# Optimization experiments

Measured on AMD Instinct MI355X. Metric: run time of the kernel, lower is better.

The kernel has to match this reference:

```python
import jax, jax.numpy as jnp
import numpy as np

N_PAPER, N_AUTHOR = 200000, 100000
D_PAPER, D_AUTHOR = 128, 64
H, OUT = 64, 32
E_CITES, E_WRITES = 4000000, 2000000


def _gcn(x, W, b, src, dst, n):
    # GCNConv with default add_self_loops=True, symmetric normalization
    xl = x @ W
    deg = jnp.zeros((n,), xl.dtype).at[dst].add(1.0) + 1.0  # +1 for self loop
    dis = jax.lax.rsqrt(deg)
    norm = dis[src] * dis[dst]
    out = jax.ops.segment_sum(xl[src] * norm[:, None], dst, num_segments=n)
    out = out + xl * (dis * dis)[:, None]  # self-loop term: norm_ii = 1/deg_i
    return out + b


def _sage(x_src, x_dst, Wl, bl, Wr, src, dst, n_dst):
    # SAGEConv: mean neighbor aggregation -> lin_l, plus root lin_r on dst
    ones = jnp.ones(src.shape, x_src.dtype)
    cnt = jnp.maximum(jax.ops.segment_sum(ones, dst, num_segments=n_dst), 1.0)
    mean = jax.ops.segment_sum(x_src[src], dst, num_segments=n_dst) / cnt[:, None]
    return mean @ Wl + bl + x_dst @ Wr


def _gat(x_src, x_dst, Ws, Wd, a_s, a_d, b, src, dst, n_dst):
    # GATConv heads=1, bipartite, add_self_loops=False, leaky_relu slope 0.2
    xs = x_src @ Ws  # [Ns, H]
    xd = x_dst @ Wd  # [Nd, H]
    a_src = xs @ a_s  # [Ns]
    a_dst = xd @ a_d  # [Nd]
    e = a_src[src] + a_dst[dst]
    e = jnp.where(e > 0, e, 0.2 * e)
    m = jax.ops.segment_max(e, dst, num_segments=n_dst)
    m = jnp.where(jnp.isfinite(m), m, 0.0)  # nodes with no in-edges
    ex = jnp.exp(e - m[dst])
    denom = jax.ops.segment_sum(ex, dst, num_segments=n_dst)
    alpha = ex / denom[dst]
    out = jax.ops.segment_sum(alpha[:, None] * xs[src], dst, num_segments=n_dst)
    return out + b


def _forward(x_paper, x_author, params, cites_src, cites_dst, writes_src, writes_dst):
    for (gW, gb, sWl, sbl, sWr, aWs, aWd, aas, aad, ab) in params:
        p_gcn = _gcn(x_paper, gW, gb, cites_src, cites_dst, N_PAPER)
        p_sage = _sage(x_author, x_paper, sWl, sbl, sWr, writes_src, writes_dst, N_PAPER)
        # rev_writes: paper -> author, i.e. src=writes_dst (paper), dst=writes_src (author)
        a_gat = _gat(x_paper, x_author, aWs, aWd, aas, aad, ab, writes_dst, writes_src, N_AUTHOR)
        x_paper = jax.nn.relu(p_gcn + p_sage)  # HeteroConv aggr='sum'
        x_author = jax.nn.relu(a_gat)
    return x_paper, x_author


def setup_inputs() -> dict:
    key = jax.random.key(0)
    ks = jax.random.split(key, 40)
    rn = lambda i, shp, s=0.1: jax.random.normal(ks[i], shp, jnp.float32) * s
    inp = {}
    inp['x_paper'] = rn(0, (N_PAPER, D_PAPER), 1.0)
    inp['x_author'] = rn(1, (N_AUTHOR, D_AUTHOR), 1.0)
    dims = [(D_PAPER, D_AUTHOR), (H, H)]
    i = 2
    for l, (dp, da) in enumerate(dims):
        inp[f'gcn_W{l}'] = rn(i, (dp, H)); i += 1
        inp[f'gcn_b{l}'] = jnp.zeros((H,), jnp.float32)
        inp[f'sage_Wl{l}'] = rn(i, (da, H)); i += 1
        inp[f'sage_bl{l}'] = jnp.zeros((H,), jnp.float32)
        inp[f'sage_Wr{l}'] = rn(i, (dp, H)); i += 1
        inp[f'gat_Ws{l}'] = rn(i, (dp, H)); i += 1
        inp[f'gat_Wd{l}'] = rn(i, (da, H)); i += 1
        inp[f'gat_as{l}'] = rn(i, (H,)); i += 1
        inp[f'gat_ad{l}'] = rn(i, (H,)); i += 1
        inp[f'gat_b{l}'] = jnp.zeros((H,), jnp.float32)
    inp['lin_W'] = rn(i, (H, OUT)); i += 1
    inp['lin_b'] = jnp.zeros((OUT,), jnp.float32)
    inp['cites_src'] = jax.random.randint(ks[30], (E_CITES,), 0, N_PAPER)
    inp['cites_dst'] = jax.random.randint(ks[31], (E_CITES,), 0, N_PAPER)
    inp['writes_src'] = jax.random.randint(ks[32], (E_WRITES,), 0, N_AUTHOR)
    inp['writes_dst'] = jax.random.randint(ks[33], (E_WRITES,), 0, N_PAPER)
    return inp


def reference(x_paper, x_author,
              gcn_W0, gcn_b0, sage_Wl0, sage_bl0, sage_Wr0,
              gat_Ws0, gat_Wd0, gat_as0, gat_ad0, gat_b0,
              gcn_W1, gcn_b1, sage_Wl1, sage_bl1, sage_Wr1,
              gat_Ws1, gat_Wd1, gat_as1, gat_ad1, gat_b1,
              lin_W, lin_b,
              cites_src, cites_dst, writes_src, writes_dst):
    params = [
        (gcn_W0, gcn_b0, sage_Wl0, sage_bl0, sage_Wr0, gat_Ws0, gat_Wd0, gat_as0, gat_ad0, gat_b0),
        (gcn_W1, gcn_b1, sage_Wl1, sage_bl1, sage_Wr1, gat_Ws1, gat_Wd1, gat_as1, gat_ad1, gat_b1),
    ]
    _, x_author_out = _forward(x_paper, x_author, params, cites_src, cites_dst, writes_src, writes_dst)
    return x_author_out @ lin_W + lin_b
```

## Files before the change

kernel.cpp:

```cpp
#include <hip/hip_runtime.h>
#include <hip/hip_bf16.h>

#define NP 200000
#define NA 100000
#define DP 128
#define HD 64
#define EC 4000000
#define EW 2000000
#define NSCAN (2 * NP + NA)
#define NBUCK 4
#define CAPC 64
#define CAPW 48
#define CAPA 64

typedef __hip_bfloat16 bf16;
typedef __attribute__((ext_vector_type(8))) short short8;
typedef __attribute__((ext_vector_type(4))) float f32x4;

__device__ __forceinline__ float bf2f(bf16 h) { return __bfloat162float(h); }

__device__ __forceinline__ short8 pack8(float4 a, float4 b) {
    union {
        short8 s;
        unsigned u[4];
    } r;
    __hip_bfloat162 h;
    h = __float22bfloat162_rn(float2{a.x, a.y});
    r.u[0] = *reinterpret_cast<unsigned*>(&h);
    h = __float22bfloat162_rn(float2{a.z, a.w});
    r.u[1] = *reinterpret_cast<unsigned*>(&h);
    h = __float22bfloat162_rn(float2{b.x, b.y});
    r.u[2] = *reinterpret_cast<unsigned*>(&h);
    h = __float22bfloat162_rn(float2{b.z, b.w});
    r.u[3] = *reinterpret_cast<unsigned*>(&h);
    return r.s;
}


__global__ __launch_bounds__(256) void fill_pass_kernel(const int* __restrict__ cs,
                                                        const int* __restrict__ cd,
                                                        const int* __restrict__ ws,
                                                        const int* __restrict__ wd,
                                                        int* __restrict__ CUR,
                                                        int* __restrict__ colC,
                                                        int* __restrict__ colWd,
                                                        int* __restrict__ colWa, int bucket) {
    long i = (long)blockIdx.x * 256 + threadIdx.x;
    if (i < EC) {
        int d = __builtin_nontemporal_load(&cd[i]);
        if ((int)(((long)d * NBUCK) / NP) != bucket) return;
        int s = __builtin_nontemporal_load(&cs[i]);
        int pos = atomicAdd(&CUR[d * 4], 1);
        if (pos < CAPC) colC[(size_t)d * CAPC + pos] = s;
    } else if (i < (long)EC + EW) {
        long e = i - EC;
        int d = __builtin_nontemporal_load(&wd[e]);
        int a = __builtin_nontemporal_load(&ws[e]);
        if ((int)(((long)d * NBUCK) / NP) == bucket) {
            int pos = atomicAdd(&CUR[(NP + d) * 4], 1);
            if (pos < CAPW) colWd[(size_t)d * CAPW + pos] = a;
        }
        if ((int)(((long)a * NBUCK) / NA) == bucket) {
            int pos = atomicAdd(&CUR[(2 * NP + a) * 4], 1);
            if (pos < CAPA) colWa[(size_t)a * CAPA + pos] = d;
        }
    }
}

__global__ __launch_bounds__(256) void finalize_kernel(const int* __restrict__ CUR,
                                                       float* __restrict__ dis,
                                                       float* __restrict__ invc) {
    int i = blockIdx.x * 256 + threadIdx.x;
    if (i >= NP) return;
    dis[i] = rsqrtf((float)CUR[i * 4] + 1.0f);
    invc[i] = 1.0f / fmaxf((float)CUR[(NP + i) * 4], 1.0f);
}


__global__ __launch_bounds__(256) void conv_author_kernel(const float* __restrict__ XA,
                                                          const float* __restrict__ wvec,
                                                          bf16* __restrict__ XAbf,
                                                          float* __restrict__ adst) {
    __shared__ float vs[64];
    if (threadIdx.x < 64) vs[threadIdx.x] = wvec[threadIdx.x];
    __syncthreads();
    int r = blockIdx.x * 4 + (threadIdx.x >> 6);
    int lane = threadIdx.x & 63;
    float x = XA[(size_t)r * 64 + lane];
    XAbf[(size_t)r * 64 + lane] = __float2bfloat16(x);
    float p = x * vs[lane];
#pragma unroll
    for (int o = 32; o > 0; o >>= 1) p += __shfl_xor(p, o, 64);
    if (lane == 0) adst[r] = p;
}


__global__ void wprep_kernel(const float* __restrict__ Wg, const float* __restrict__ Wl,
                             const float* __restrict__ Wr, const float* __restrict__ Ws0,
                             const float* __restrict__ Ws1, short* __restrict__ WF,
                             const float* __restrict__ Wd0, const float* __restrict__ ad0,
                             const float* __restrict__ Wd1, const float* __restrict__ ad1,
                             float* __restrict__ wvec0, float* __restrict__ wvec1) {
    int bid = blockIdx.x;
    int lane = threadIdx.x;
    if (bid >= 64) {
        const float* Wd = (bid == 64) ? Wd0 : Wd1;
        const float* ad = (bid == 64) ? ad0 : ad1;
        float* wv = (bid == 64) ? wvec0 : wvec1;
        float s = 0.f;
        for (int c = 0; c < 64; c++) s += Wd[lane * 64 + c] * ad[c];
        wv[lane] = s;
        return;
    }
    int q = lane & 15, g = lane >> 4;
    int m, r;
    size_t dst;
    if (bid < 16) {
        m = 0; r = bid; dst = 0;
    } else if (bid < 40) {
        m = 1; r = bid - 16; dst = 8192;
    } else if (bid < 56) {
        m = 2; r = bid - 40; dst = 20480;
    } else {
        m = 3; r = bid - 56; dst = 28672;
    }
    int ks = r >> 2, n = r & 3;
    int col = n * 16 + q;
    float v[8];
#pragma unroll
    for (int j = 0; j < 8; j++) {
        int kr = ks * 32 + g * 8 + j;
        float x;
        if (m == 0) x = Wg[(size_t)kr * 64 + col];
        else if (m == 1) x = (kr < 64) ? Wl[(size_t)kr * 64 + col] : Wr[(size_t)(kr - 64) * 64 + col];
        else if (m == 2) x = Ws0[(size_t)kr * 64 + col];
        else x = Ws1[(size_t)kr * 64 + col];
        v[j] = x;
    }
    short8 s = pack8(float4{v[0], v[1], v[2], v[3]}, float4{v[4], v[5], v[6], v[7]});
    *reinterpret_cast<short8*>(WF + dst + ((size_t)r * 64 + lane) * 8) = s;
}


template <int K, int ASTRIDE, bool ABF16, bool ADOT, bool SCALE>
__global__ __launch_bounds__(256) void mfma_gemm_kernel(const void* __restrict__ Xv,
                                                        const short* __restrict__ Wf,
                                                        bf16* __restrict__ outb,
                                                        const float* __restrict__ avec,
                                                        float* __restrict__ adot,
                                                        const float* __restrict__ rowscale) {
    int tid = threadIdx.x;
    int lane = tid & 63, q = lane & 15, g = lane >> 4;
    int rw = blockIdx.x * 64 + (tid >> 6) * 16;
    int arow = rw + q;
    f32x4 acc[4];
#pragma unroll
    for (int n = 0; n < 4; n++) acc[n] = f32x4{0.f, 0.f, 0.f, 0.f};
#pragma unroll
    for (int ks = 0; ks < K / 32; ks++) {
        short8 af;
        if constexpr (ABF16) {
            af = *reinterpret_cast<const short8*>((const bf16*)Xv + (size_t)arow * ASTRIDE +
                                                  ks * 32 + g * 8);
        } else {
            const float* xr = (const float*)Xv + (size_t)arow * ASTRIDE + ks * 32 + g * 8;
            float4 a0 = *reinterpret_cast<const float4*>(xr);
            float4 a1 = *reinterpret_cast<const float4*>(xr + 4);
            af = pack8(a0, a1);
        }
#pragma unroll
        for (int n = 0; n < 4; n++) {
            short8 bfr =
                *reinterpret_cast<const short8*>(Wf + ((size_t)(ks * 4 + n) * 64 + lane) * 8);
            acc[n] = __builtin_amdgcn_mfma_f32_16x16x32_bf16(af, bfr, acc[n], 0, 0, 0);
        }
    }
    float av[4];
    if constexpr (ADOT) {
#pragma unroll
        for (int n = 0; n < 4; n++) av[n] = avec[n * 16 + q];
    }
#pragma unroll
    for (int j = 0; j < 4; j++) {
        int R = rw + g * 4 + j;
        float sc = 1.f;
        if constexpr (SCALE) sc = rowscale[R];
#pragma unroll
        for (int n = 0; n < 4; n++) {
            outb[(size_t)R * 64 + n * 16 + q] = __float2bfloat16(acc[n][j] * sc);
        }
        if constexpr (ADOT) {
            float t = acc[0][j] * av[0] + acc[1][j] * av[1] + acc[2][j] * av[2] + acc[3][j] * av[3];
            t += __shfl_xor(t, 1, 64);
            t += __shfl_xor(t, 2, 64);
            t += __shfl_xor(t, 4, 64);
            t += __shfl_xor(t, 8, 64);
            if (q == 0) adot[R] = t;
        }
    }
}


__global__ __launch_bounds__(256) void mfma_sage_kernel(const bf16* B3s,
                                                        const float* __restrict__ XP,
                                                        const float* __restrict__ B2,
                                                        const float* __restrict__ bl,
                                                        const short* __restrict__ Wf, bf16* P1) {
    int tid = threadIdx.x;
    int lane = tid & 63, q = lane & 15, g = lane >> 4;
    int rw = blockIdx.x * 64 + (tid >> 6) * 16;
    int arow = rw + q;
    f32x4 acc[4];
#pragma unroll
    for (int n = 0; n < 4; n++) acc[n] = f32x4{0.f, 0.f, 0.f, 0.f};
#pragma unroll
    for (int ks = 0; ks < 6; ks++) {
        short8 af;
        if (ks < 2) {
            af = *reinterpret_cast<const short8*>(B3s + (size_t)arow * 128 + 64 + ks * 32 + g * 8);
        } else {
            const float* xr = XP + (size_t)arow * DP + (ks - 2) * 32 + g * 8;
            float4 a0 = *reinterpret_cast<const float4*>(xr);
            float4 a1 = *reinterpret_cast<const float4*>(xr + 4);
            af = pack8(a0, a1);
        }
#pragma unroll
        for (int n = 0; n < 4; n++) {
            short8 bfr =
                *reinterpret_cast<const short8*>(Wf + ((size_t)(ks * 4 + n) * 64 + lane) * 8);
            acc[n] = __builtin_amdgcn_mfma_f32_16x16x32_bf16(af, bfr, acc[n], 0, 0, 0);
        }
    }
    float blv[4];
#pragma unroll
    for (int n = 0; n < 4; n++) blv[n] = bl[n * 16 + q];
#pragma unroll
    for (int j = 0; j < 4; j++) {
        int R = rw + g * 4 + j;
#pragma unroll
        for (int n = 0; n < 4; n++) {
            int col = n * 16 + q;
            float v = acc[n][j] + B2[(size_t)R * 64 + col] + blv[n];
            P1[(size_t)R * 128 + col] = __float2bfloat16(fmaxf(v, 0.f));
        }
    }
}


__global__ __launch_bounds__(256) void paper_gather_kernel(const bf16* __restrict__ B1,
                                                           const bf16* __restrict__ XA,
                                                           const int* __restrict__ CUR,
                                                           const int* colC,
                                                           const int* __restrict__ colWd,
                                                           const float* __restrict__ dis,
                                                           const float* __restrict__ invc,
                                                           const float* __restrict__ gb,
                                                           float* __restrict__ B2, bf16* B3s) {
    int node = __builtin_amdgcn_readfirstlane(blockIdx.x * 4 + (threadIdx.x >> 6));
    unsigned lane = threadIdx.x & 63;
    int degc = min(CUR[(unsigned)node * 4], CAPC);
    unsigned cb = (unsigned)node * CAPC;
    float dd = dis[(unsigned)node];
    float acc = bf2f(B1[((unsigned)node << 6) + lane]);
    int e = 0;
    for (; e + 8 <= degc; e += 8) {
        unsigned off[8];
#pragma unroll
        for (int j = 0; j < 8; j++) off[j] = ((unsigned)colC[cb + e + j] << 6) + lane;
        float v[8];
#pragma unroll
        for (int j = 0; j < 8; j++) v[j] = bf2f(B1[off[j]]);
#pragma unroll
        for (int j = 0; j < 8; j++) acc += v[j];
    }
    for (; e + 4 <= degc; e += 4) {
        unsigned o0 = ((unsigned)colC[cb + e] << 6) + lane;
        unsigned o1 = ((unsigned)colC[cb + e + 1] << 6) + lane;
        unsigned o2 = ((unsigned)colC[cb + e + 2] << 6) + lane;
        unsigned o3 = ((unsigned)colC[cb + e + 3] << 6) + lane;
        float v0 = bf2f(B1[o0]), v1 = bf2f(B1[o1]);
        float v2 = bf2f(B1[o2]), v3 = bf2f(B1[o3]);
        acc += v0 + v1;
        acc += v2 + v3;
    }
    for (; e < degc; e++) acc += bf2f(B1[((unsigned)colC[cb + e] << 6) + lane]);
    B2[((unsigned)node << 6) + lane] = acc * dd + gb[lane];
    int degw = min(CUR[((unsigned)NP + node) * 4], CAPW);
    unsigned wb = (unsigned)node * CAPW;
    float s = 0.f;
    e = 0;
    for (; e + 8 <= degw; e += 8) {
        unsigned off[8];
#pragma unroll
        for (int j = 0; j < 8; j++) off[j] = ((unsigned)colWd[wb + e + j] << 6) + lane;
        float v[8];
#pragma unroll
        for (int j = 0; j < 8; j++) v[j] = bf2f(XA[off[j]]);
#pragma unroll
        for (int j = 0; j < 8; j++) s += v[j];
    }
    for (; e + 4 <= degw; e += 4) {
        unsigned o0 = ((unsigned)colWd[wb + e] << 6) + lane;
        unsigned o1 = ((unsigned)colWd[wb + e + 1] << 6) + lane;
        unsigned o2 = ((unsigned)colWd[wb + e + 2] << 6) + lane;
        unsigned o3 = ((unsigned)colWd[wb + e + 3] << 6) + lane;
        float v0 = bf2f(XA[o0]), v1 = bf2f(XA[o1]);
        float v2 = bf2f(XA[o2]), v3 = bf2f(XA[o3]);
        s += v0 + v1;
        s += v2 + v3;
    }
    for (; e < degw; e++) s += bf2f(XA[((unsigned)colWd[wb + e] << 6) + lane]);
    B3s[(unsigned)node * 128u + 64u + lane] = __float2bfloat16(s * invc[(unsigned)node]);
}


__device__ __forceinline__ float lrelu(float v) { return v > 0.f ? v : 0.2f * v; }


__global__ __launch_bounds__(256) void gat_l0_kernel(const bf16* __restrict__ XS,
                                                     const int* __restrict__ CUR,
                                                     const int* __restrict__ colA,
                                                     const float* __restrict__ asrc,
                                                     float* __restrict__ adst,
                                                     const float* __restrict__ ab,
                                                     const float* __restrict__ wvec1) {
    int a = __builtin_amdgcn_readfirstlane(blockIdx.x * 4 + (threadIdx.x >> 6));
    unsigned lane = threadIdx.x & 63;
    int deg = min(CUR[(2u * NP + a) * 4], CAPA);
    unsigned cb = (unsigned)a * CAPA;
    float ada = adst[(unsigned)a];
    float acc = 0.f, den = 0.f;
    int e = 0;
    for (; e + 8 <= deg; e += 8) {
        unsigned p[8];
#pragma unroll
        for (int j = 0; j < 8; j++) p[j] = (unsigned)colA[cb + e + j];
        float x[8], v[8];
#pragma unroll
        for (int j = 0; j < 8; j++) x[j] = __expf(lrelu(asrc[p[j]] + ada));
#pragma unroll
        for (int j = 0; j < 8; j++) v[j] = bf2f(XS[(p[j] << 6) + lane]);
#pragma unroll
        for (int j = 0; j < 8; j++) {
            den += x[j];
            acc += x[j] * v[j];
        }
    }
    for (; e + 4 <= deg; e += 4) {
        unsigned p0 = (unsigned)colA[cb + e], p1 = (unsigned)colA[cb + e + 1];
        unsigned p2 = (unsigned)colA[cb + e + 2], p3 = (unsigned)colA[cb + e + 3];
        float x0 = __expf(lrelu(asrc[p0] + ada));
        float x1 = __expf(lrelu(asrc[p1] + ada));
        float x2 = __expf(lrelu(asrc[p2] + ada));
        float x3 = __expf(lrelu(asrc[p3] + ada));
        den += (x0 + x1) + (x2 + x3);
        acc += x0 * bf2f(XS[(p0 << 6) + lane]);
        acc += x1 * bf2f(XS[(p1 << 6) + lane]);
        acc += x2 * bf2f(XS[(p2 << 6) + lane]);
        acc += x3 * bf2f(XS[(p3 << 6) + lane]);
    }
    for (; e < deg; e++) {
        unsigned p = (unsigned)colA[cb + e];
        float x = __expf(lrelu(asrc[p] + ada));
        den += x;
        acc += x * bf2f(XS[(p << 6) + lane]);
    }
    float inv = den > 0.f ? 1.f / den : 0.f;
    float val = fmaxf(acc * inv + ab[lane], 0.f);
    float pr = val * wvec1[lane];
#pragma unroll
    for (int o = 32; o > 0; o >>= 1) pr += __shfl_xor(pr, o, 64);
    if (lane == 0) adst[(unsigned)a] = pr;
}


__global__ __launch_bounds__(256) void gat_final_kernel(const bf16* __restrict__ XS,
                                                        const int* __restrict__ CUR,
                                                        const int* __restrict__ colA,
                                                        const float* __restrict__ asrc,
                                                        const float* __restrict__ adst,
                                                        const float* __restrict__ ab,
                                                        const float* __restrict__ linW,
                                                        const float* __restrict__ linb,
                                                        float* __restrict__ out) {
    __shared__ float Ws[64 * 32];
    __shared__ float vbuf[4][64];
    __shared__ float lbs[32];
    int tid = threadIdx.x;
    for (int i = tid; i < 64 * 32; i += 256) Ws[i] = linW[i];
    if (tid < 32) lbs[tid] = linb[tid];
    __syncthreads();
    int wid = tid >> 6;
    int a = __builtin_amdgcn_readfirstlane(blockIdx.x * 4 + wid);
    unsigned lane = tid & 63;
    int deg = min(CUR[(2u * NP + a) * 4], CAPA);
    unsigned cb = (unsigned)a * CAPA;
    float ada = adst[(unsigned)a];
    float acc = 0.f, den = 0.f;
    int e = 0;
    for (; e + 8 <= deg; e += 8) {
        unsigned p[8];
#pragma unroll
        for (int j = 0; j < 8; j++) p[j] = (unsigned)colA[cb + e + j];
        float x[8], v[8];
#pragma unroll
        for (int j = 0; j < 8; j++) x[j] = __expf(lrelu(asrc[p[j]] + ada));
#pragma unroll
        for (int j = 0; j < 8; j++) v[j] = bf2f(XS[(p[j] << 6) + lane]);
#pragma unroll
        for (int j = 0; j < 8; j++) {
            den += x[j];
            acc += x[j] * v[j];
        }
    }
    for (; e + 4 <= deg; e += 4) {
        unsigned p0 = (unsigned)colA[cb + e], p1 = (unsigned)colA[cb + e + 1];
        unsigned p2 = (unsigned)colA[cb + e + 2], p3 = (unsigned)colA[cb + e + 3];
        float x0 = __expf(lrelu(asrc[p0] + ada));
        float x1 = __expf(lrelu(asrc[p1] + ada));
        float x2 = __expf(lrelu(asrc[p2] + ada));
        float x3 = __expf(lrelu(asrc[p3] + ada));
        den += (x0 + x1) + (x2 + x3);
        acc += x0 * bf2f(XS[(p0 << 6) + lane]);
        acc += x1 * bf2f(XS[(p1 << 6) + lane]);
        acc += x2 * bf2f(XS[(p2 << 6) + lane]);
        acc += x3 * bf2f(XS[(p3 << 6) + lane]);
    }
    for (; e < deg; e++) {
        unsigned p = (unsigned)colA[cb + e];
        float x = __expf(lrelu(asrc[p] + ada));
        den += x;
        acc += x * bf2f(XS[(p << 6) + lane]);
    }
    float inv = den > 0.f ? 1.f / den : 0.f;
    vbuf[wid][lane] = fmaxf(acc * inv + ab[lane], 0.f);
    __syncthreads();
    if (tid < 128) {
        int w = tid >> 5, c = tid & 31;
        int node = blockIdx.x * 4 + w;
        float s = lbs[c];
#pragma unroll
        for (int k = 0; k < 64; k++) s += vbuf[w][k] * Ws[k * 32 + c];
        out[(size_t)node * 32 + c] = s;
    }
}


static inline int cdivi(long a, long b) { return (int)((a + b - 1) / b); }

extern "C" void kernel_launch(void* const* d_in, const int* in_sizes, int n_in, void* d_out,
                              int out_size, void* d_ws, size_t ws_size, hipStream_t stream) {
    const float* x_paper = (const float*)d_in[0];
    const float* x_author = (const float*)d_in[1];
    const float* gcn_W0 = (const float*)d_in[2];
    const float* gcn_b0 = (const float*)d_in[3];
    const float* sage_Wl0 = (const float*)d_in[4];
    const float* sage_bl0 = (const float*)d_in[5];
    const float* sage_Wr0 = (const float*)d_in[6];
    const float* gat_Ws0 = (const float*)d_in[7];
    const float* gat_Wd0 = (const float*)d_in[8];
    const float* gat_as0 = (const float*)d_in[9];
    const float* gat_ad0 = (const float*)d_in[10];
    const float* gat_b0 = (const float*)d_in[11];
    const float* gat_Ws1 = (const float*)d_in[17];
    const float* gat_Wd1 = (const float*)d_in[18];
    const float* gat_as1 = (const float*)d_in[19];
    const float* gat_ad1 = (const float*)d_in[20];
    const float* gat_b1 = (const float*)d_in[21];
    const float* lin_W = (const float*)d_in[22];
    const float* lin_b = (const float*)d_in[23];
    const int* cites_src = (const int*)d_in[24];
    const int* cites_dst = (const int*)d_in[25];
    const int* writes_src = (const int*)d_in[26];
    const int* writes_dst = (const int*)d_in[27];

    float* out = (float*)d_out;

    char* base = (char*)d_ws;
    bf16* BF = (bf16*)base;
    base += (size_t)NP * 64 * 2;
    float* B2 = (float*)base;
    base += (size_t)NP * 64 * 4;
    int* colC = (int*)base;
    bf16* R3 = (bf16*)base;
    base += (size_t)NP * CAPC * 4;
    int* colWd = (int*)base;
    base += (size_t)NP * CAPW * 4;
    int* colWa = (int*)base;
    base += (size_t)NA * CAPA * 4;
    bf16* XAbf = (bf16*)base;
    base += (size_t)NA * 64 * 2;
    int* CUR = (int*)base;
    base += (size_t)NSCAN * 4 * 4;
    float* dis_p = (float*)base;
    float* invc = dis_p + NP;
    float* asrc = invc + NP;
    float* adst = asrc + NP;
    float* wvec0 = adst + NA;
    float* wvec1 = wvec0 + 64;
    short* WF = (short*)(wvec1 + 64);

    dim3 blk(256);
    const long EMERGED = (long)EC + EW;

    hipMemsetAsync(CUR, 0, (size_t)NSCAN * 4 * 4, stream);
    wprep_kernel<<<66, 64, 0, stream>>>(gcn_W0, sage_Wl0, sage_Wr0, gat_Ws0, gat_Ws1, WF, gat_Wd0,
                                        gat_ad0, gat_Wd1, gat_ad1, wvec0, wvec1);

    for (int b = 0; b < NBUCK; b++) {
        fill_pass_kernel<<<cdivi(EMERGED, 256), blk, 0, stream>>>(cites_src, cites_dst,
                                                                  writes_src, writes_dst, CUR,
                                                                  colC, colWd, colWa, b);
    }
    finalize_kernel<<<cdivi(NP, 256), blk, 0, stream>>>(CUR, dis_p, invc);

    conv_author_kernel<<<NA / 4, blk, 0, stream>>>(x_author, wvec0, XAbf, adst);

    mfma_gemm_kernel<DP, DP, false, false, true><<<NP / 64, blk, 0, stream>>>(x_paper, WF, BF,
                                                                              nullptr, nullptr,
                                                                              dis_p);
    paper_gather_kernel<<<NP / 4, blk, 0, stream>>>(BF, XAbf, CUR, colC, colWd, dis_p, invc,
                                                    gcn_b0, B2, R3);

    mfma_sage_kernel<<<NP / 64, blk, 0, stream>>>(R3, x_paper, B2, sage_bl0, WF + 8192, R3);

    mfma_gemm_kernel<DP, DP, false, true, false><<<NP / 64, blk, 0, stream>>>(
        x_paper, WF + 20480, BF, gat_as0, asrc, nullptr);
    gat_l0_kernel<<<NA / 4, blk, 0, stream>>>(BF, CUR, colWa, asrc, adst, gat_b0, wvec1);

    mfma_gemm_kernel<HD, 128, true, true, false><<<NP / 64, blk, 0, stream>>>(
        R3, WF + 28672, BF, gat_as1, asrc, nullptr);
    gat_final_kernel<<<NA / 4, blk, 0, stream>>>(BF, CUR, colWa, asrc, adst, gat_b1, lin_W, lin_b,
                                                 out);
}
```

Before: 842.5 us.

## Fuse two GAT layers into one kernel and inline degree normalization

Removes the finalize kernel: the GCN scale and SAGE inverse count are now computed inline from the degree counters in the GEMM epilogue and the paper gather kernel. Both GAT layer projections now run before a single fused kernel that performs layer-0 attention, computes the layer-1 destination score in registers, then runs layer-1 attention and the final linear. The layer-1 projected features go to a separate buffer that reuses the colWd region, so the author adjacency list is walked in one launch. This saves two launches and an adst round trip, in exchange for keeping two feature buffers live and a longer kernel.

```diff
diff --git a/kernel.cpp b/kernel.cpp
--- a/kernel.cpp
+++ b/kernel.cpp
@@ -67,15 +67,6 @@
     }
 }
 
-__global__ __launch_bounds__(256) void finalize_kernel(const int* __restrict__ CUR,
-                                                       float* __restrict__ dis,
-                                                       float* __restrict__ invc) {
-    int i = blockIdx.x * 256 + threadIdx.x;
-    if (i >= NP) return;
-    dis[i] = rsqrtf((float)CUR[i * 4] + 1.0f);
-    invc[i] = 1.0f / fmaxf((float)CUR[(NP + i) * 4], 1.0f);
-}
-
 
 __global__ __launch_bounds__(256) void conv_author_kernel(const float* __restrict__ XA,
                                                           const float* __restrict__ wvec,
@@ -148,7 +139,7 @@
                                                         bf16* __restrict__ outb,
                                                         const float* __restrict__ avec,
                                                         float* __restrict__ adot,
-                                                        const float* __restrict__ rowscale) {
+                                                        const int* __restrict__ CURs) {
     int tid = threadIdx.x;
     int lane = tid & 63, q = lane & 15, g = lane >> 4;
     int rw = blockIdx.x * 64 + (tid >> 6) * 16;
@@ -184,7 +175,7 @@
     for (int j = 0; j < 4; j++) {
         int R = rw + g * 4 + j;
         float sc = 1.f;
-        if constexpr (SCALE) sc = rowscale[R];
+        if constexpr (SCALE) sc = rsqrtf((float)CURs[(unsigned)R * 4] + 1.0f);
 #pragma unroll
         for (int n = 0; n < 4; n++) {
             outb[(size_t)R * 64 + n * 16 + q] = __float2bfloat16(acc[n][j] * sc);
@@ -252,15 +243,14 @@
                                                            const int* __restrict__ CUR,
                                                            const int* colC,
                                                            const int* __restrict__ colWd,
-                                                           const float* __restrict__ dis,
-                                                           const float* __restrict__ invc,
                                                            const float* __restrict__ gb,
                                                            float* __restrict__ B2, bf16* B3s) {
     int node = __builtin_amdgcn_readfirstlane(blockIdx.x * 4 + (threadIdx.x >> 6));
     unsigned lane = threadIdx.x & 63;
-    int degc = min(CUR[(unsigned)node * 4], CAPC);
+    int degc_t = CUR[(unsigned)node * 4];
+    float dd = rsqrtf((float)degc_t + 1.0f);
+    int degc = min(degc_t, CAPC);
     unsigned cb = (unsigned)node * CAPC;
-    float dd = dis[(unsigned)node];
     float acc = bf2f(B1[((unsigned)node << 6) + lane]);
     int e = 0;
     for (; e + 8 <= degc; e += 8) {
@@ -285,7 +275,9 @@
     }
     for (; e < degc; e++) acc += bf2f(B1[((unsigned)colC[cb + e] << 6) + lane]);
     B2[((unsigned)node << 6) + lane] = acc * dd + gb[lane];
-    int degw = min(CUR[((unsigned)NP + node) * 4], CAPW);
+    int degw_t = CUR[((unsigned)NP + node) * 4];
+    float ic = 1.0f / fmaxf((float)degw_t, 1.0f);
+    int degw = min(degw_t, CAPW);
     unsigned wb = (unsigned)node * CAPW;
     float s = 0.f;
     e = 0;
@@ -310,25 +302,16 @@
         s += v2 + v3;
     }
     for (; e < degw; e++) s += bf2f(XA[((unsigned)colWd[wb + e] << 6) + lane]);
-    B3s[(unsigned)node * 128u + 64u + lane] = __float2bfloat16(s * invc[(unsigned)node]);
+    B3s[(unsigned)node * 128u + 64u + lane] = __float2bfloat16(s * ic);
 }
 
 
 __device__ __forceinline__ float lrelu(float v) { return v > 0.f ? v : 0.2f * v; }
 
-
-__global__ __launch_bounds__(256) void gat_l0_kernel(const bf16* __restrict__ XS,
-                                                     const int* __restrict__ CUR,
-                                                     const int* __restrict__ colA,
-                                                     const float* __restrict__ asrc,
-                                                     float* __restrict__ adst,
-                                                     const float* __restrict__ ab,
-                                                     const float* __restrict__ wvec1) {
-    int a = __builtin_amdgcn_readfirstlane(blockIdx.x * 4 + (threadIdx.x >> 6));
-    unsigned lane = threadIdx.x & 63;
-    int deg = min(CUR[(2u * NP + a) * 4], CAPA);
-    unsigned cb = (unsigned)a * CAPA;
-    float ada = adst[(unsigned)a];
+__device__ __forceinline__ void gat_phase(const bf16* __restrict__ XS,
+                                          const float* __restrict__ asrc, const int* __restrict__ colA,
+                                          unsigned cb, int deg, float ada, unsigned lane,
+                                          float& accO, float& denO) {
     float acc = 0.f, den = 0.f;
     int e = 0;
     for (; e + 8 <= deg; e += 8) {
@@ -365,24 +348,17 @@
         den += x;
         acc += x * bf2f(XS[(p << 6) + lane]);
     }
-    float inv = den > 0.f ? 1.f / den : 0.f;
-    float val = fmaxf(acc * inv + ab[lane], 0.f);
-    float pr = val * wvec1[lane];
-#pragma unroll
-    for (int o = 32; o > 0; o >>= 1) pr += __shfl_xor(pr, o, 64);
-    if (lane == 0) adst[(unsigned)a] = pr;
-}
-
-
-__global__ __launch_bounds__(256) void gat_final_kernel(const bf16* __restrict__ XS,
-                                                        const int* __restrict__ CUR,
-                                                        const int* __restrict__ colA,
-                                                        const float* __restrict__ asrc,
-                                                        const float* __restrict__ adst,
-                                                        const float* __restrict__ ab,
-                                                        const float* __restrict__ linW,
-                                                        const float* __restrict__ linb,
-                                                        float* __restrict__ out) {
+    accO = acc;
+    denO = den;
+}
+
+__global__ __launch_bounds__(256) void gat_fused_kernel(
+    const bf16* __restrict__ XS0, const bf16* __restrict__ XS1, const int* __restrict__ CUR,
+    const int* __restrict__ colA, const float* __restrict__ asrc0,
+    const float* __restrict__ asrc1, const float* __restrict__ adst0,
+    const float* __restrict__ ab0, const float* __restrict__ wvec1,
+    const float* __restrict__ ab1, const float* __restrict__ linW,
+    const float* __restrict__ linb, float* __restrict__ out) {
     __shared__ float Ws[64 * 32];
     __shared__ float vbuf[4][64];
     __shared__ float lbs[32];
@@ -395,45 +371,17 @@
     unsigned lane = tid & 63;
     int deg = min(CUR[(2u * NP + a) * 4], CAPA);
     unsigned cb = (unsigned)a * CAPA;
-    float ada = adst[(unsigned)a];
-    float acc = 0.f, den = 0.f;
-    int e = 0;
-    for (; e + 8 <= deg; e += 8) {
-        unsigned p[8];
-#pragma unroll
-        for (int j = 0; j < 8; j++) p[j] = (unsigned)colA[cb + e + j];
-        float x[8], v[8];
-#pragma unroll
-        for (int j = 0; j < 8; j++) x[j] = __expf(lrelu(asrc[p[j]] + ada));
-#pragma unroll
-        for (int j = 0; j < 8; j++) v[j] = bf2f(XS[(p[j] << 6) + lane]);
-#pragma unroll
-        for (int j = 0; j < 8; j++) {
-            den += x[j];
-            acc += x[j] * v[j];
-        }
-    }
-    for (; e + 4 <= deg; e += 4) {
-        unsigned p0 = (unsigned)colA[cb + e], p1 = (unsigned)colA[cb + e + 1];
-        unsigned p2 = (unsigned)colA[cb + e + 2], p3 = (unsigned)colA[cb + e + 3];
-        float x0 = __expf(lrelu(asrc[p0] + ada));
-        float x1 = __expf(lrelu(asrc[p1] + ada));
-        float x2 = __expf(lrelu(asrc[p2] + ada));
-        float x3 = __expf(lrelu(asrc[p3] + ada));
-        den += (x0 + x1) + (x2 + x3);
-        acc += x0 * bf2f(XS[(p0 << 6) + lane]);
-        acc += x1 * bf2f(XS[(p1 << 6) + lane]);
-        acc += x2 * bf2f(XS[(p2 << 6) + lane]);
-        acc += x3 * bf2f(XS[(p3 << 6) + lane]);
-    }
-    for (; e < deg; e++) {
-        unsigned p = (unsigned)colA[cb + e];
-        float x = __expf(lrelu(asrc[p] + ada));
-        den += x;
-        acc += x * bf2f(XS[(p << 6) + lane]);
-    }
-    float inv = den > 0.f ? 1.f / den : 0.f;
-    vbuf[wid][lane] = fmaxf(acc * inv + ab[lane], 0.f);
+    float acc0, den0;
+    gat_phase(XS0, asrc0, colA, cb, deg, adst0[(unsigned)a], lane, acc0, den0);
+    float inv0 = den0 > 0.f ? 1.f / den0 : 0.f;
+    float val0 = fmaxf(acc0 * inv0 + ab0[lane], 0.f);
+    float ada1 = val0 * wvec1[lane];
+#pragma unroll
+    for (int o = 32; o > 0; o >>= 1) ada1 += __shfl_xor(ada1, o, 64);
+    float acc1, den1;
+    gat_phase(XS1, asrc1, colA, cb, deg, ada1, lane, acc1, den1);
+    float inv1 = den1 > 0.f ? 1.f / den1 : 0.f;
+    vbuf[wid][lane] = fmaxf(acc1 * inv1 + ab1[lane], 0.f);
     __syncthreads();
     if (tid < 128) {
         int w = tid >> 5, c = tid & 31;
@@ -485,6 +433,7 @@
     bf16* R3 = (bf16*)base;
     base += (size_t)NP * CAPC * 4;
     int* colWd = (int*)base;
+    bf16* XS1 = (bf16*)base;
     base += (size_t)NP * CAPW * 4;
     int* colWa = (int*)base;
     base += (size_t)NA * CAPA * 4;
@@ -492,11 +441,10 @@
     base += (size_t)NA * 64 * 2;
     int* CUR = (int*)base;
     base += (size_t)NSCAN * 4 * 4;
-    float* dis_p = (float*)base;
-    float* invc = dis_p + NP;
-    float* asrc = invc + NP;
-    float* adst = asrc + NP;
-    float* wvec0 = adst + NA;
+    float* asrc0 = (float*)base;
+    float* asrc1 = asrc0 + NP;
+    float* adst0 = asrc1 + NP;
+    float* wvec0 = adst0 + NA;
     float* wvec1 = wvec0 + 64;
     short* WF = (short*)(wvec1 + 64);
 
@@ -512,24 +460,21 @@
                                                                   writes_src, writes_dst, CUR,
                                                                   colC, colWd, colWa, b);
     }
-    finalize_kernel<<<cdivi(NP, 256), blk, 0, stream>>>(CUR, dis_p, invc);
-
-    conv_author_kernel<<<NA / 4, blk, 0, stream>>>(x_author, wvec0, XAbf, adst);
+
+    conv_author_kernel<<<NA / 4, blk, 0, stream>>>(x_author, wvec0, XAbf, adst0);
 
     mfma_gemm_kernel<DP, DP, false, false, true><<<NP / 64, blk, 0, stream>>>(x_paper, WF, BF,
                                                                               nullptr, nullptr,
-                                                                              dis_p);
-    paper_gather_kernel<<<NP / 4, blk, 0, stream>>>(BF, XAbf, CUR, colC, colWd, dis_p, invc,
-                                                    gcn_b0, B2, R3);
+                                                                              CUR);
+    paper_gather_kernel<<<NP / 4, blk, 0, stream>>>(BF, XAbf, CUR, colC, colWd, gcn_b0, B2, R3);
 
     mfma_sage_kernel<<<NP / 64, blk, 0, stream>>>(R3, x_paper, B2, sage_bl0, WF + 8192, R3);
 
     mfma_gemm_kernel<DP, DP, false, true, false><<<NP / 64, blk, 0, stream>>>(
-        x_paper, WF + 20480, BF, gat_as0, asrc, nullptr);
-    gat_l0_kernel<<<NA / 4, blk, 0, stream>>>(BF, CUR, colWa, asrc, adst, gat_b0, wvec1);
-
+        x_paper, WF + 20480, BF, gat_as0, asrc0, nullptr);
     mfma_gemm_kernel<HD, 128, true, true, false><<<NP / 64, blk, 0, stream>>>(
-        R3, WF + 28672, BF, gat_as1, asrc, nullptr);
-    gat_final_kernel<<<NA / 4, blk, 0, stream>>>(BF, CUR, colWa, asrc, adst, gat_b1, lin_W, lin_b,
-                                                 out);
-}
+        R3, WF + 28672, XS1, gat_as1, asrc1, nullptr);
+
+    gat_fused_kernel<<<NA / 4, blk, 0, stream>>>(BF, XS1, CUR, colWa, asrc0, asrc1, adst0, gat_b0,
+                                                 wvec1, gat_b1, lin_W, lin_b, out);
+}
```

New measurement: 817.1 us. -3.0%, faster.
